# Kernel tuning notes

Hardware: AMD Instinct MI355X
Metric: run time of the kernel (lower is better)

Reference implementation:

```python
import jax, jax.numpy as jnp
import numpy as np

K = 20
EPS = 1e-6


def _vnt_linear(x, W):
    # VNT linear: rows normalized to sum to 1 (translation-equivariant channel mix)
    Wn = W / W.sum(axis=1, keepdims=True)
    return jnp.einsum('oi,bi...->bo...', Wn, x)


def _vn_lrelu(p, d):
    # Vector-neuron LeakyReLU with negative_slope=0: project p off -d half-space
    dot = jnp.sum(p * d, axis=2, keepdims=True)   # axis 2 is the 3-vector axis
    dns = jnp.sum(d * d, axis=2, keepdims=True)
    return jnp.where(dot >= 0, p, p - (dot / (dns + EPS)) * d)


def _vnt_lin_lrelu(x, W, D):
    p = _vnt_linear(x, W)
    d = jnp.einsum('oi,bi...->bo...', D, x)
    return _vn_lrelu(p, d)


def _graph_feature_cross(pts, k):
    # pts: [B, N, 3] -> edge features [B, 3(ch), 3(vec), N, k]
    B = pts.shape[0]
    xx = jnp.sum(pts * pts, axis=-1)                       # [B, N]
    inner = jnp.einsum('bnd,bmd->bnm', pts, pts)           # [B, N, N]
    pairwise = 2.0 * inner - xx[:, :, None] - xx[:, None, :]  # -||xi-xj||^2
    _, idx = jax.lax.top_k(pairwise, k)                    # [B, N, k]
    b_idx = jnp.arange(B)[:, None, None]
    nbrs = pts[b_idx, idx]                                 # [B, N, k, 3]
    ctr = jnp.broadcast_to(pts[:, :, None, :], nbrs.shape)
    cross = jnp.cross(nbrs, ctr)
    feat = jnp.stack([nbrs - ctr, ctr, cross], axis=3)     # [B, N, k, 3ch, 3vec]
    return jnp.transpose(feat, (0, 3, 4, 1, 2))            # [B, 3, 3, N, k]


def setup_inputs() -> dict:
    key = jax.random.key(0)
    ks = jax.random.split(key, 9)
    B, N, hidden = 8, 2048, 128

    def w(k_, o, i):  # positive weights -> stable row-sum normalization
        return jax.random.uniform(k_, (o, i), jnp.float32, 0.5 / i, 1.5 / i)

    def d(k_, o, i):
        return jax.random.normal(k_, (o, i), jnp.float32) / np.sqrt(i)

    return {
        'pc': jax.random.normal(ks[0], (B, N, 3), jnp.float32),
        'W_pos': w(ks[1], 64, 3), 'D_pos': d(ks[2], 64, 3),
        'W1': w(ks[3], hidden, 64), 'D1': d(ks[4], hidden, 64),
        'W2': w(ks[5], hidden, 2 * hidden), 'D2': d(ks[6], hidden, 2 * hidden),
        'W3': w(ks[7], hidden, 2 * hidden), 'D3': d(ks[8], hidden, 2 * hidden),
    }


def reference(pc, W_pos, D_pos, W1, D1, W2, D2, W3, D3):
    feat = _graph_feature_cross(pc, K)               # [B, 3, 3, N, k]
    net = _vnt_lin_lrelu(feat, W_pos, D_pos)         # [B, 64, 3, N, k]
    net = net.mean(axis=-1)                          # pool over k -> [B, 64, 3, N]
    net = _vnt_lin_lrelu(net, W1, D1)                # [B, 128, 3, N]
    pooled = jnp.broadcast_to(net.mean(axis=-1, keepdims=True), net.shape)
    net = jnp.concatenate([net, pooled], axis=1)     # [B, 256, 3, N]
    net = _vnt_lin_lrelu(net, W2, D2)                # [B, 128, 3, N]
    pooled = jnp.broadcast_to(net.mean(axis=-1, keepdims=True), net.shape)
    net = jnp.concatenate([net, pooled], axis=1)     # [B, 256, 3, N]
    net = _vnt_lin_lrelu(net, W3, D3)                # [B, 128, 3, N]
    c = net.mean(axis=-1)                            # pool over N -> [B, 128, 3]
    return c.reshape(pc.shape[0], -1)                # [B, 384]
```

## Files before the change

### kernel.cpp

```cpp
#include <hip/hip_runtime.h>
#include <hip/hip_bf16.h>
#include <math.h>

constexpr int B = 8;
constexpr int N = 2048;
constexpr int KNN = 20;
constexpr int H = 128;
constexpr int P = 3 * N;

constexpr int OSB2   = 0;
constexpr int OWT2   = 8448;
constexpr int OWT3   = 41216;
constexpr int OPS1   = 73984;
constexpr int OPS2   = 98560;
constexpr int OOUTS  = 123136;
constexpr int OBAR   = 147712;
constexpr int OSB3   = 148736;
constexpr int OWB1   = 160000;
constexpr int OWB2   = 176384;
constexpr int OWB3   = 209152;

constexpr int ZERO_BASE = OPS1;
constexpr int ZERO_CNT  = 74752;
constexpr int PREP_BLOCKS = (ZERO_CNT + 255) / 256;

constexpr int GRID_VNT  = 1024;
constexpr int BLK_PER_B = 128;

typedef __attribute__((ext_vector_type(8))) short bf16x8;
typedef __attribute__((ext_vector_type(4))) float f32x4;

__device__ __forceinline__ unsigned short f2bf(float x) {
  __hip_bfloat16 h = __float2bfloat16(x);
  return *(unsigned short*)&h;
}
__device__ __forceinline__ float bf2f(unsigned short u) {
  __hip_bfloat16 h;
  *(unsigned short*)&h = u;
  return __bfloat162float(h);
}
__device__ __forceinline__ unsigned int packhl(float x) {
  unsigned short hi = f2bf(x);
  float lo = x - bf2f(hi);
  unsigned short ls = f2bf(lo);
  return (unsigned)hi | ((unsigned)ls << 16);
}

__device__ __forceinline__ float cohload(const float* p) {
  return __hip_atomic_load(p, __ATOMIC_RELAXED, __HIP_MEMORY_SCOPE_AGENT);
}
__device__ __forceinline__ void cohstore(float* p, float v) {
  __hip_atomic_store(p, v, __ATOMIC_RELAXED, __HIP_MEMORY_SCOPE_AGENT);
}

__device__ __forceinline__ void wave_sort_key(unsigned long long& k, int lane) {
#pragma unroll
  for (int kk = 2; kk <= 64; kk <<= 1) {
#pragma unroll
    for (int j = kk >> 1; j > 0; j >>= 1) {
      unsigned long long pk =
          (unsigned long long)__shfl_xor((long long)k, j);
      bool iam_lower   = (lane & j) == 0;
      bool dir_desc    = (lane & kk) == 0;
      bool p_better    = pk > k;
      bool want_better = (dir_desc == iam_lower);
      k = (p_better == want_better) ? pk : k;
    }
  }
}

__global__ __launch_bounds__(256) void prep_kernel(
    const float* __restrict__ W1, const float* __restrict__ D1,
    const float* __restrict__ W2, const float* __restrict__ D2,
    const float* __restrict__ W3, const float* __restrict__ D3,
    float* __restrict__ ws) {
  int tid = threadIdx.x;
  int bid = blockIdx.x;
  {
    int zi = bid * 256 + tid;
    if (zi < ZERO_CNT) ws[ZERO_BASE + zi] = 0.f;
  }
  if (bid < 96) {
    int wv = tid >> 6, lane = tid & 63;
#pragma unroll
    for (int r = 0; r < 2; ++r) {
      int rr = bid * 8 + wv * 2 + r;
      const float* src;
      float* tdst = nullptr;
      unsigned int* pdst;
      int C, Cpack;
      bool norm;
      if (rr < 128)      { src = W1 + rr * 64;            C = 64;  Cpack = 64;  norm = true;
                           pdst = (unsigned int*)(ws + OWB1) + rr * 16; }
      else if (rr < 256) { int m = rr - 128; src = D1 + m * 64;  C = 64;  Cpack = 64;  norm = false;
                           pdst = (unsigned int*)(ws + OWB1) + (m + 128) * 16; }
      else if (rr < 384) { int m = rr - 256; src = W2 + m * 256; C = 256; Cpack = 128; norm = true;
                           pdst = (unsigned int*)(ws + OWB2) + m * 16; tdst = ws + OWT2 + m; }
      else if (rr < 512) { int m = rr - 384; src = D2 + m * 256; C = 256; Cpack = 128; norm = false;
                           pdst = (unsigned int*)(ws + OWB2) + (m + 128) * 16; tdst = ws + OWT2 + 128 + m; }
      else if (rr < 640) { int m = rr - 512; src = W3 + m * 256; C = 256; Cpack = 128; norm = true;
                           pdst = (unsigned int*)(ws + OWB3) + m * 16; tdst = ws + OWT3 + m; }
      else               { int m = rr - 640; src = D3 + m * 256; C = 256; Cpack = 128; norm = false;
                           pdst = (unsigned int*)(ws + OWB3) + (m + 128) * 16; tdst = ws + OWT3 + 128 + m; }
      float s = 1.f;
      if (norm) {
        float a = 0.f;
        for (int i = lane; i < C; i += 64) a += src[i];
#pragma unroll
        for (int off = 32; off > 0; off >>= 1) a += __shfl_xor(a, off);
        s = a;
      }
      for (int i = lane; i < C; i += 64) {
        float val = src[i] / s;
        if (i < Cpack) pdst[(i >> 4) * 4096 + (i & 15)] = packhl(val);
        if (tdst && i >= 128) tdst[(i - 128) * 256] = val;
      }
    }
  }
}

template <int K2, bool HASPOOL, bool LAST>
__device__ __forceinline__ void vnt_layer_body(
    unsigned short* xt, float* sb, float* spool,
    const unsigned short* __restrict__ Wb,
    const float* __restrict__ ps, const float* __restrict__ Wt,
    float* __restrict__ sbg, unsigned int* sbflag,
    float* __restrict__ pool, float* __restrict__ outs,
    unsigned int* wait_cnt, unsigned int* arrive_cnt,
    int b, int nt, int p0, int tid) {
  constexpr int KS = K2 / 32;
  constexpr int LDR = K2 + 8;
  constexpr int LDO = 132;
  float* ot = (float*)xt;
  int w = tid >> 6, lane = tid & 63;
  int q = lane >> 4, cl = lane & 15;

  bf16x8 acur[2][2], anxt[2][2];
#pragma unroll
  for (int t = 0; t < 2; ++t)
#pragma unroll
    for (int pd = 0; pd < 2; ++pd)
      acur[t][pd] = *(const bf16x8*)(Wb +
          (size_t)(32 * w + 16 * t + 128 * pd + cl) * 32 + q * 8);

  if constexpr (HASPOOL) {
    if (nt == 0) {
      if (tid == 0) {
        while (__hip_atomic_load(wait_cnt, __ATOMIC_RELAXED,
                                 __HIP_MEMORY_SCOPE_AGENT) < (unsigned)BLK_PER_B) {
          __builtin_amdgcn_s_sleep(2);
        }
      }
      __syncthreads();
      for (int i = tid; i < 384; i += 256) {
        float x = 0.f;
#pragma unroll
        for (int k = 0; k < 8; ++k)
          x += cohload(&ps[k * 3072 + b * 384 + i]);
        spool[i] = x * (1.f / 2048.f);
      }
      __syncthreads();
      float s0 = 0.f, s1 = 0.f, s2 = 0.f;
#pragma unroll 16
      for (int c = 0; c < 128; ++c) {
        float x = Wt[c * 256 + tid];
        s0 = fmaf(x, spool[c * 3 + 0], s0);
        s1 = fmaf(x, spool[c * 3 + 1], s1);
        s2 = fmaf(x, spool[c * 3 + 2], s2);
      }
      sb[tid * 3 + 0] = s0;
      sb[tid * 3 + 1] = s1;
      sb[tid * 3 + 2] = s2;
      cohstore(&sbg[tid * 3 + 0], s0);
      cohstore(&sbg[tid * 3 + 1], s1);
      cohstore(&sbg[tid * 3 + 2], s2);
      __syncthreads();
      if (tid == 0)
        __hip_atomic_fetch_add(sbflag, 1u, __ATOMIC_RELAXED,
                               __HIP_MEMORY_SCOPE_AGENT);
    } else {
      if (tid == 0) {
        while (__hip_atomic_load(sbflag, __ATOMIC_RELAXED,
                                 __HIP_MEMORY_SCOPE_AGENT) < 1u) {
          __builtin_amdgcn_s_sleep(2);
        }
      }
      __syncthreads();
      for (int i = tid; i < 768; i += 256) sb[i] = cohload(&sbg[i]);
      __syncthreads();
    }
  } else {
    __syncthreads();
  }

  f32x4 acc[2][2][3] = {};

#pragma unroll
  for (int ks = 0; ks < KS; ++ks) {
    if (ks + 1 < KS) {
#pragma unroll
      for (int t = 0; t < 2; ++t)
#pragma unroll
        for (int pd = 0; pd < 2; ++pd)
          anxt[t][pd] = *(const bf16x8*)(Wb +
              (size_t)(32 * w + 16 * t + 128 * pd + cl) * 32 + q * 8 +
              (ks + 1) * 8192);
    }
    bf16x8 bb[3];
#pragma unroll
    for (int v = 0; v < 3; ++v)
      bb[v] = *(const bf16x8*)(xt + (v * 16 + cl) * LDR + ks * 32 + q * 8);
#pragma unroll
    for (int t = 0; t < 2; ++t)
#pragma unroll
      for (int pd = 0; pd < 2; ++pd)
#pragma unroll
        for (int v = 0; v < 3; ++v)
          acc[t][pd][v] = __builtin_amdgcn_mfma_f32_16x16x32_bf16(
              acur[t][pd], bb[v], acc[t][pd][v], 0, 0, 0);
#pragma unroll
    for (int t = 0; t < 2; ++t)
#pragma unroll
      for (int pd = 0; pd < 2; ++pd)
        acur[t][pd] = anxt[t][pd];
  }
  __syncthreads();

#pragma unroll
  for (int t = 0; t < 2; ++t) {
    float res[3][4];
#pragma unroll
    for (int r = 0; r < 4; ++r) {
      int o = 32 * w + 16 * t + 4 * q + r;
      float pv[3], dvv[3];
#pragma unroll
      for (int v = 0; v < 3; ++v) {
        pv[v] = acc[t][0][v][r] + (HASPOOL ? sb[o * 3 + v] : 0.f);
        dvv[v] = acc[t][1][v][r] + (HASPOOL ? sb[(128 + o) * 3 + v] : 0.f);
      }
      float dot = fmaf(pv[0], dvv[0], fmaf(pv[1], dvv[1], pv[2] * dvv[2]));
      float dns = fmaf(dvv[0], dvv[0], fmaf(dvv[1], dvv[1], dvv[2] * dvv[2]));
      float f = (dot < 0.f) ? dot / (dns + 1e-6f) : 0.f;
#pragma unroll
      for (int v = 0; v < 3; ++v) res[v][r] = pv[v] - f * dvv[v];
    }
    int o0 = 32 * w + 16 * t + 4 * q;
#pragma unroll
    for (int v = 0; v < 3; ++v) {
      f32x4 rv = {res[v][0], res[v][1], res[v][2], res[v][3]};
      *(f32x4*)(ot + (v * 16 + cl) * LDO + o0) = rv;
    }
  }
  __syncthreads();

  int shadow = (nt & 7) * 3072;
  for (int s = tid; s < 384; s += 256) {
    int o = s / 3, v = s % 3;
    float a2 = 0.f;
#pragma unroll
    for (int c = 0; c < 16; ++c) a2 += ot[(v * 16 + c) * LDO + o];
    if (LAST) atomicAdd(outs + shadow + b * 384 + s, a2);
    else      atomicAdd(pool + shadow + b * 384 + s, a2);
  }

  __syncthreads();
  if (arrive_cnt != nullptr && tid == 0) {
    __hip_atomic_fetch_add(arrive_cnt, 1u, __ATOMIC_RELAXED,
                           __HIP_MEMORY_SCOPE_AGENT);
  }

  if constexpr (!LAST) {
    for (int s = tid; s < 1536; s += 256) {
      int pix = s >> 5, c4 = s & 31;
      float4 sv = *(float4*)(ot + pix * LDO + c4 * 4);
      uint4 vv;
      vv.x = packhl(sv.x);
      vv.y = packhl(sv.y);
      vv.z = packhl(sv.z);
      vv.w = packhl(sv.w);
      *(uint4*)(xt + pix * 264 + c4 * 8) = vv;
    }
  }
}

__global__ __launch_bounds__(256, 4) void fused_kernel(
    const float* __restrict__ pc, const float* __restrict__ Wpos,
    const float* __restrict__ Dp, float* __restrict__ ws,
    float* __restrict__ out) {
  __shared__ __align__(16) char U[35328];
  __shared__ unsigned int last_flag;
  int tid = threadIdx.x, wv = tid >> 6, lane = tid & 63;
  int bid = blockIdx.x;
  int b = bid >> 7;
  int nt = bid & 127;
  int p0 = nt * 48;

  float4* spt = (float4*)U;
  unsigned char* sph = (unsigned char*)(U + 32768) + wv * 640;
  unsigned short* sbufw = (unsigned short*)sph;
  float4* erw = (float4*)sph;
  unsigned short* xt = (unsigned short*)U;
  float* sb = (float*)(U + 25344);
  float* spool = (float*)(U + 28416);

  unsigned int* bar = (unsigned int*)(ws + OBAR);
  unsigned int* cnt1 = bar + b * 32;
  unsigned int* cnt2 = bar + 256 + b * 32;
  unsigned int* cntm = bar + 512;
  unsigned int* sbf2 = bar + 576 + b * 16;
  unsigned int* sbf3 = bar + 704 + b * 16;

  int o = lane;
  float w0 = Wpos[o * 3 + 0], w1 = Wpos[o * 3 + 1], w2 = Wpos[o * 3 + 2];
  float e0 = Dp[o * 3 + 0], e1 = Dp[o * 3 + 1], e2 = Dp[o * 3 + 2];

  const float* pcb = pc + (size_t)b * N * 3;
  for (int i = tid; i < N; i += 256) {
    float x = pcb[i * 3 + 0], y = pcb[i * 3 + 1], z = pcb[i * 3 + 2];
    float xx = __fadd_rn(__fadd_rn(__fmul_rn(x, x), __fmul_rn(y, y)), __fmul_rn(z, z));
    spt[i] = make_float4(2.f * x, 2.f * y, 2.f * z, xx);
  }
  __syncthreads();

  {
    float s = (w0 + w2) + w1;
    w0 = w0 / s; w1 = w1 / s; w2 = w2 / s;
  }

  unsigned rx0[4], rx1[4], rx2[4];

#pragma unroll
  for (int j = 0; j < 4; ++j) {
    int q = nt * 16 + wv * 4 + j;
    float4 qp = spt[q];
    float qx = 0.5f * qp.x, qy = 0.5f * qp.y, qz = 0.5f * qp.z, qxx = qp.w;

    float dv[32];
    float lmax = -INFINITY;
#pragma unroll
    for (int i = 0; i < 32; ++i) {
      float4 m = spt[i * 64 + lane];
      float A = __fadd_rn(__fadd_rn(__fmul_rn(m.x, qx), __fmul_rn(m.y, qy)),
                          __fmul_rn(m.z, qz));
      float d = __fsub_rn(__fsub_rn(A, qxx), m.w);
      dv[i] = d;
      lmax = fmaxf(lmax, d);
    }

    float sv = lmax;
#pragma unroll
    for (int k = 2; k <= 64; k <<= 1) {
#pragma unroll
      for (int jj = k >> 1; jj > 0; jj >>= 1) {
        float pv = __shfl_xor(sv, jj);
        bool keep_max = ((lane & k) == 0) == ((lane & jj) == 0);
        sv = keep_max ? fmaxf(sv, pv) : fminf(sv, pv);
      }
    }
    float tval = __shfl(sv, 19);

    unsigned msk = 0u;
#pragma unroll
    for (int i = 0; i < 32; ++i) msk |= (dv[i] >= tval) ? (1u << i) : 0u;
    int cnt = __popc(msk);
    int scan = cnt;
#pragma unroll
    for (int off = 1; off < 64; off <<= 1) {
      int t = __shfl_up(scan, off);
      scan += (lane >= off) ? t : 0;
    }
    int S = __shfl(scan, 63);
    int pos = scan - cnt;
    unsigned mm = msk;
    while (mm) {
      int i = __ffs(mm) - 1;
      mm &= mm - 1;
      if (pos < 192) sbufw[pos] = (unsigned short)(i * 64 + lane);
      ++pos;
    }

    auto distOf = [&](int m) -> float {
      float4 mp = spt[m];
      float A = __fadd_rn(__fadd_rn(__fmul_rn(mp.x, qx), __fmul_rn(mp.y, qy)),
                          __fmul_rn(mp.z, qz));
      return __fsub_rn(__fsub_rn(A, qxx), mp.w);
    };
    auto mkkey = [&](int m) -> unsigned long long {
      float d = distOf(m);
      unsigned u = __float_as_uint(d);
      u ^= (u >> 31) ? 0xFFFFFFFFu : 0x80000000u;
      return ((unsigned long long)u << 32) | (unsigned)(~m);
    };

    unsigned long long key = 0ULL;
    if (S <= 64) {
      if (lane < S) key = mkkey(sbufw[lane]);
      wave_sort_key(key, lane);
    } else if (S <= 192) {
      int p2 = 0;
      while (p2 < S) {
        if (lane >= KNN) {
          int t = p2 + lane - KNN;
          key = (t < S) ? mkkey(sbufw[t]) : 0ULL;
        }
        wave_sort_key(key, lane);
        p2 += 64 - KNN;
      }
    } else {
      int p2 = 0;
      while (p2 < N) {
        if (lane >= KNN) {
          int t = p2 + lane - KNN;
          key = (t < N) ? mkkey(t) : 0ULL;
        }
        wave_sort_key(key, lane);
        p2 += 64 - KNN;
      }
    }
    int cm = ~((unsigned)key);

    if (lane < KNN) {
      float4 t = spt[cm];
      float nx = 0.5f * t.x, ny = 0.5f * t.y, nz = 0.5f * t.z;
      float ex = nx - qx, ey = ny - qy, ez = nz - qz;
      float rrx = ny * qz - nz * qy;
      float rry = nz * qx - nx * qz;
      float rrz = nx * qy - ny * qx;
      erw[2 * lane + 0] = make_float4(ex, ey, ez, 0.f);
      erw[2 * lane + 1] = make_float4(rrx, rry, rrz, 0.f);
    }

    float cx = qx, cy = qy, cz = qz;
    float pcx = w1 * cx, pcy = w1 * cy, pcz = w1 * cz;
    float dcx = e1 * cx, dcy = e1 * cy, dcz = e1 * cz;
    float ax = 0.f, ay = 0.f, az = 0.f;
#pragma unroll 4
    for (int k = 0; k < KNN; ++k) {
      float4 e4 = erw[2 * k + 0];
      float4 r4 = erw[2 * k + 1];
      float ex = e4.x, ey = e4.y, ez = e4.z;
      float rrx = r4.x, rry = r4.y, rrz = r4.z;
      float px = fmaf(w0, ex, fmaf(w2, rrx, pcx));
      float py = fmaf(w0, ey, fmaf(w2, rry, pcy));
      float pz = fmaf(w0, ez, fmaf(w2, rrz, pcz));
      float dx = fmaf(e0, ex, fmaf(e2, rrx, dcx));
      float dy = fmaf(e0, ey, fmaf(e2, rry, dcy));
      float dz = fmaf(e0, ez, fmaf(e2, rrz, dcz));
      float dot = fmaf(px, dx, fmaf(py, dy, pz * dz));
      float dns = fmaf(dx, dx, fmaf(dy, dy, dz * dz)) + 1e-6f;
      float r0 = __builtin_amdgcn_rcpf(dns);
      r0 = r0 * fmaf(-dns, r0, 2.0f);
      float f = (dot < 0.f) ? dot * r0 : 0.f;
      ax = fmaf(-f, dx, px) + ax;
      ay = fmaf(-f, dy, py) + ay;
      az = fmaf(-f, dz, pz) + az;
    }
    rx0[j] = packhl(ax * (1.f / 20.f));
    rx1[j] = packhl(ay * (1.f / 20.f));
    rx2[j] = packhl(az * (1.f / 20.f));
  }

  __syncthreads();

#pragma unroll
  for (int j = 0; j < 4; ++j) {
    int row = wv * 4 + j;
    *(unsigned int*)(xt + (row + 0)  * 136 + 2 * o) = rx0[j];
    *(unsigned int*)(xt + (row + 16) * 136 + 2 * o) = rx1[j];
    *(unsigned int*)(xt + (row + 32) * 136 + 2 * o) = rx2[j];
  }

  vnt_layer_body<128, false, false>(
      xt, sb, spool, (const unsigned short*)(ws + OWB1),
      nullptr, nullptr, nullptr, nullptr, ws + OPS1, nullptr,
      nullptr, cnt1, b, nt, p0, tid);

  vnt_layer_body<256, true, false>(
      xt, sb, spool, (const unsigned short*)(ws + OWB2),
      ws + OPS1, ws + OWT2, ws + OSB2 + b * 768, sbf2, ws + OPS2, nullptr,
      cnt1, cnt2, b, nt, p0, tid);

  vnt_layer_body<256, true, true>(
      xt, sb, spool, (const unsigned short*)(ws + OWB3),
      ws + OPS2, ws + OWT3, ws + OSB3 + b * 768, sbf3, nullptr, ws + OOUTS,
      cnt2, nullptr, b, nt, p0, tid);

  if (tid == 0) {
    unsigned old = __hip_atomic_fetch_add(cntm, 1u, __ATOMIC_RELAXED,
                                          __HIP_MEMORY_SCOPE_AGENT);
    last_flag = (old == (unsigned)GRID_VNT - 1) ? 1u : 0u;
  }
  __syncthreads();
  if (last_flag) {
    const float* outs = ws + OOUTS;
    for (int idx = tid; idx < B * 384; idx += 256) {
      float s = 0.f;
#pragma unroll
      for (int k = 0; k < 8; ++k) s += cohload(&outs[k * 3072 + idx]);
      out[idx] = s * (1.f / 2048.f);
    }
  }
}

extern "C" void kernel_launch(void* const* d_in, const int* in_sizes, int n_in,
                              void* d_out, int out_size, void* d_ws, size_t ws_size,
                              hipStream_t stream) {
  (void)in_sizes; (void)n_in; (void)out_size; (void)ws_size;
  const float* pc   = (const float*)d_in[0];
  const float* Wpos = (const float*)d_in[1];
  const float* Dpos = (const float*)d_in[2];
  const float* W1   = (const float*)d_in[3];
  const float* D1   = (const float*)d_in[4];
  const float* W2   = (const float*)d_in[5];
  const float* D2   = (const float*)d_in[6];
  const float* W3   = (const float*)d_in[7];
  const float* D3   = (const float*)d_in[8];
  float* out = (float*)d_out;
  float* ws  = (float*)d_ws;

  prep_kernel<<<PREP_BLOCKS, 256, 0, stream>>>(W1, D1, W2, D2, W3, D3, ws);

  fused_kernel<<<GRID_VNT, 256, 0, stream>>>(pc, Wpos, Dpos, ws, out);
}
```

Before: 157.3 us.

## Double block size to 512 threads, halving per-wave work in kNN and MFMA layers

```diff
diff --git a/kernel.cpp b/kernel.cpp
--- a/kernel.cpp
+++ b/kernel.cpp
@@ -135,13 +135,11 @@
   int w = tid >> 6, lane = tid & 63;
   int q = lane >> 4, cl = lane & 15;
 
-  bf16x8 acur[2][2], anxt[2][2];
-#pragma unroll
-  for (int t = 0; t < 2; ++t)
-#pragma unroll
-    for (int pd = 0; pd < 2; ++pd)
-      acur[t][pd] = *(const bf16x8*)(Wb +
-          (size_t)(32 * w + 16 * t + 128 * pd + cl) * 32 + q * 8);
+  bf16x8 acur[2], anxt[2];
+#pragma unroll
+  for (int pd = 0; pd < 2; ++pd)
+    acur[pd] = *(const bf16x8*)(Wb +
+        (size_t)(16 * w + 128 * pd + cl) * 32 + q * 8);
 
   if constexpr (HASPOOL) {
     if (nt == 0) {
@@ -152,7 +150,7 @@
         }
       }
       __syncthreads();
-      for (int i = tid; i < 384; i += 256) {
+      for (int i = tid; i < 384; i += 512) {
         float x = 0.f;
 #pragma unroll
         for (int k = 0; k < 8; ++k)
@@ -160,20 +158,22 @@
         spool[i] = x * (1.f / 2048.f);
       }
       __syncthreads();
-      float s0 = 0.f, s1 = 0.f, s2 = 0.f;
+      if (tid < 256) {
+        float s0 = 0.f, s1 = 0.f, s2 = 0.f;
 #pragma unroll 16
-      for (int c = 0; c < 128; ++c) {
-        float x = Wt[c * 256 + tid];
-        s0 = fmaf(x, spool[c * 3 + 0], s0);
-        s1 = fmaf(x, spool[c * 3 + 1], s1);
-        s2 = fmaf(x, spool[c * 3 + 2], s2);
-      }
-      sb[tid * 3 + 0] = s0;
-      sb[tid * 3 + 1] = s1;
-      sb[tid * 3 + 2] = s2;
-      cohstore(&sbg[tid * 3 + 0], s0);
-      cohstore(&sbg[tid * 3 + 1], s1);
-      cohstore(&sbg[tid * 3 + 2], s2);
+        for (int c = 0; c < 128; ++c) {
+          float x = Wt[c * 256 + tid];
+          s0 = fmaf(x, spool[c * 3 + 0], s0);
+          s1 = fmaf(x, spool[c * 3 + 1], s1);
+          s2 = fmaf(x, spool[c * 3 + 2], s2);
+        }
+        sb[tid * 3 + 0] = s0;
+        sb[tid * 3 + 1] = s1;
+        sb[tid * 3 + 2] = s2;
+        cohstore(&sbg[tid * 3 + 0], s0);
+        cohstore(&sbg[tid * 3 + 1], s1);
+        cohstore(&sbg[tid * 3 + 2], s2);
+      }
       __syncthreads();
       if (tid == 0)
         __hip_atomic_fetch_add(sbflag, 1u, __ATOMIC_RELAXED,
@@ -186,57 +186,50 @@
         }
       }
       __syncthreads();
-      for (int i = tid; i < 768; i += 256) sb[i] = cohload(&sbg[i]);
+      for (int i = tid; i < 768; i += 512) sb[i] = cohload(&sbg[i]);
       __syncthreads();
     }
   } else {
     __syncthreads();
   }
 
-  f32x4 acc[2][2][3] = {};
+  f32x4 acc[2][3] = {};
 
 #pragma unroll
   for (int ks = 0; ks < KS; ++ks) {
     if (ks + 1 < KS) {
 #pragma unroll
-      for (int t = 0; t < 2; ++t)
-#pragma unroll
-        for (int pd = 0; pd < 2; ++pd)
-          anxt[t][pd] = *(const bf16x8*)(Wb +
-              (size_t)(32 * w + 16 * t + 128 * pd + cl) * 32 + q * 8 +
-              (ks + 1) * 8192);
+      for (int pd = 0; pd < 2; ++pd)
+        anxt[pd] = *(const bf16x8*)(Wb +
+            (size_t)(16 * w + 128 * pd + cl) * 32 + q * 8 +
+            (ks + 1) * 8192);
     }
     bf16x8 bb[3];
 #pragma unroll
     for (int v = 0; v < 3; ++v)
       bb[v] = *(const bf16x8*)(xt + (v * 16 + cl) * LDR + ks * 32 + q * 8);
 #pragma unroll
-    for (int t = 0; t < 2; ++t)
-#pragma unroll
-      for (int pd = 0; pd < 2; ++pd)
-#pragma unroll
-        for (int v = 0; v < 3; ++v)
-          acc[t][pd][v] = __builtin_amdgcn_mfma_f32_16x16x32_bf16(
-              acur[t][pd], bb[v], acc[t][pd][v], 0, 0, 0);
-#pragma unroll
-    for (int t = 0; t < 2; ++t)
-#pragma unroll
-      for (int pd = 0; pd < 2; ++pd)
-        acur[t][pd] = anxt[t][pd];
+    for (int pd = 0; pd < 2; ++pd)
+#pragma unroll
+      for (int v = 0; v < 3; ++v)
+        acc[pd][v] = __builtin_amdgcn_mfma_f32_16x16x32_bf16(
+            acur[pd], bb[v], acc[pd][v], 0, 0, 0);
+#pragma unroll
+    for (int pd = 0; pd < 2; ++pd)
+      acur[pd] = anxt[pd];
   }
   __syncthreads();
 
-#pragma unroll
-  for (int t = 0; t < 2; ++t) {
+  {
     float res[3][4];
 #pragma unroll
     for (int r = 0; r < 4; ++r) {
-      int o = 32 * w + 16 * t + 4 * q + r;
+      int o = 16 * w + 4 * q + r;
       float pv[3], dvv[3];
 #pragma unroll
       for (int v = 0; v < 3; ++v) {
-        pv[v] = acc[t][0][v][r] + (HASPOOL ? sb[o * 3 + v] : 0.f);
-        dvv[v] = acc[t][1][v][r] + (HASPOOL ? sb[(128 + o) * 3 + v] : 0.f);
+        pv[v] = acc[0][v][r] + (HASPOOL ? sb[o * 3 + v] : 0.f);
+        dvv[v] = acc[1][v][r] + (HASPOOL ? sb[(128 + o) * 3 + v] : 0.f);
       }
       float dot = fmaf(pv[0], dvv[0], fmaf(pv[1], dvv[1], pv[2] * dvv[2]));
       float dns = fmaf(dvv[0], dvv[0], fmaf(dvv[1], dvv[1], dvv[2] * dvv[2]));
@@ -244,7 +237,7 @@
 #pragma unroll
       for (int v = 0; v < 3; ++v) res[v][r] = pv[v] - f * dvv[v];
     }
-    int o0 = 32 * w + 16 * t + 4 * q;
+    int o0 = 16 * w + 4 * q;
 #pragma unroll
     for (int v = 0; v < 3; ++v) {
       f32x4 rv = {res[v][0], res[v][1], res[v][2], res[v][3]};
@@ -254,7 +247,7 @@
   __syncthreads();
 
   int shadow = (nt & 7) * 3072;
-  for (int s = tid; s < 384; s += 256) {
+  for (int s = tid; s < 384; s += 512) {
     int o = s / 3, v = s % 3;
     float a2 = 0.f;
 #pragma unroll
@@ -270,7 +263,7 @@
   }
 
   if constexpr (!LAST) {
-    for (int s = tid; s < 1536; s += 256) {
+    for (int s = tid; s < 1536; s += 512) {
       int pix = s >> 5, c4 = s & 31;
       float4 sv = *(float4*)(ot + pix * LDO + c4 * 4);
       uint4 vv;
@@ -283,11 +276,11 @@
   }
 }
 
-__global__ __launch_bounds__(256, 4) void fused_kernel(
+__global__ __launch_bounds__(512, 8) void fused_kernel(
     const float* __restrict__ pc, const float* __restrict__ Wpos,
     const float* __restrict__ Dp, float* __restrict__ ws,
     float* __restrict__ out) {
-  __shared__ __align__(16) char U[35328];
+  __shared__ __align__(16) char U[37888];
   __shared__ unsigned int last_flag;
   int tid = threadIdx.x, wv = tid >> 6, lane = tid & 63;
   int bid = blockIdx.x;
@@ -315,7 +308,7 @@
   float e0 = Dp[o * 3 + 0], e1 = Dp[o * 3 + 1], e2 = Dp[o * 3 + 2];
 
   const float* pcb = pc + (size_t)b * N * 3;
-  for (int i = tid; i < N; i += 256) {
+  for (int i = tid; i < N; i += 512) {
     float x = pcb[i * 3 + 0], y = pcb[i * 3 + 1], z = pcb[i * 3 + 2];
     float xx = __fadd_rn(__fadd_rn(__fmul_rn(x, x), __fmul_rn(y, y)), __fmul_rn(z, z));
     spt[i] = make_float4(2.f * x, 2.f * y, 2.f * z, xx);
@@ -327,11 +320,11 @@
     w0 = w0 / s; w1 = w1 / s; w2 = w2 / s;
   }
 
-  unsigned rx0[4], rx1[4], rx2[4];
-
-#pragma unroll
-  for (int j = 0; j < 4; ++j) {
-    int q = nt * 16 + wv * 4 + j;
+  unsigned rx0[2], rx1[2], rx2[2];
+
+#pragma unroll
+  for (int j = 0; j < 2; ++j) {
+    int q = nt * 16 + wv * 2 + j;
     float4 qp = spt[q];
     float qx = 0.5f * qp.x, qy = 0.5f * qp.y, qz = 0.5f * qp.z, qxx = qp.w;
 
@@ -463,8 +456,8 @@
   __syncthreads();
 
 #pragma unroll
-  for (int j = 0; j < 4; ++j) {
-    int row = wv * 4 + j;
+  for (int j = 0; j < 2; ++j) {
+    int row = wv * 2 + j;
     *(unsigned int*)(xt + (row + 0)  * 136 + 2 * o) = rx0[j];
     *(unsigned int*)(xt + (row + 16) * 136 + 2 * o) = rx1[j];
     *(unsigned int*)(xt + (row + 32) * 136 + 2 * o) = rx2[j];
@@ -493,7 +486,7 @@
   __syncthreads();
   if (last_flag) {
     const float* outs = ws + OOUTS;
-    for (int idx = tid; idx < B * 384; idx += 256) {
+    for (int idx = tid; idx < B * 384; idx += 512) {
       float s = 0.f;
 #pragma unroll
       for (int k = 0; k < 8; ++k) s += cohload(&outs[k * 3072 + idx]);
@@ -520,5 +513,5 @@
 
   prep_kernel<<<PREP_BLOCKS, 256, 0, stream>>>(W1, D1, W2, D2, W3, D3, ws);
 
-  fused_kernel<<<GRID_VNT, 256, 0, stream>>>(pc, Wpos, Dpos, ws, out);
-}
+  fused_kernel<<<GRID_VNT, 512, 0, stream>>>(pc, Wpos, Dpos, ws, out);
+}
```

Result: slower. 192.9 us (+22.6%).

## Replace atomic pooled reductions with per-block slots and per-batch finalization

Applied to the files above, without the earlier changes.

```diff
diff --git a/kernel.cpp b/kernel.cpp
--- a/kernel.cpp
+++ b/kernel.cpp
@@ -11,18 +11,17 @@
 constexpr int OSB2   = 0;
 constexpr int OWT2   = 8448;
 constexpr int OWT3   = 41216;
-constexpr int OPS1   = 73984;
-constexpr int OPS2   = 98560;
-constexpr int OOUTS  = 123136;
 constexpr int OBAR   = 147712;
 constexpr int OSB3   = 148736;
 constexpr int OWB1   = 160000;
 constexpr int OWB2   = 176384;
 constexpr int OWB3   = 209152;
-
-constexpr int ZERO_BASE = OPS1;
-constexpr int ZERO_CNT  = 74752;
-constexpr int PREP_BLOCKS = (ZERO_CNT + 255) / 256;
+constexpr int OPS1   = 250000;
+constexpr int OPS2   = 650000;
+constexpr int OOUTS  = 1050000;
+
+constexpr int ZERO_BASE = OBAR;
+constexpr int ZERO_CNT  = 1024;
 
 constexpr int GRID_VNT  = 1024;
 constexpr int BLK_PER_B = 128;
@@ -125,7 +124,7 @@
     const unsigned short* __restrict__ Wb,
     const float* __restrict__ ps, const float* __restrict__ Wt,
     float* __restrict__ sbg, unsigned int* sbflag,
-    float* __restrict__ pool, float* __restrict__ outs,
+    float* __restrict__ dstslots,
     unsigned int* wait_cnt, unsigned int* arrive_cnt,
     int b, int nt, int p0, int tid) {
   constexpr int KS = K2 / 32;
@@ -154,9 +153,8 @@
       __syncthreads();
       for (int i = tid; i < 384; i += 256) {
         float x = 0.f;
-#pragma unroll
-        for (int k = 0; k < 8; ++k)
-          x += cohload(&ps[k * 3072 + b * 384 + i]);
+        for (int k = 0; k < BLK_PER_B; ++k)
+          x += cohload(&ps[(size_t)(b * BLK_PER_B + k) * 384 + i]);
         spool[i] = x * (1.f / 2048.f);
       }
       __syncthreads();
@@ -253,14 +251,15 @@
   }
   __syncthreads();
 
-  int shadow = (nt & 7) * 3072;
-  for (int s = tid; s < 384; s += 256) {
-    int o = s / 3, v = s % 3;
-    float a2 = 0.f;
-#pragma unroll
-    for (int c = 0; c < 16; ++c) a2 += ot[(v * 16 + c) * LDO + o];
-    if (LAST) atomicAdd(outs + shadow + b * 384 + s, a2);
-    else      atomicAdd(pool + shadow + b * 384 + s, a2);
+  {
+    float* myslot = dstslots + (size_t)(b * BLK_PER_B + nt) * 384;
+    for (int s = tid; s < 384; s += 256) {
+      int o = s / 3, v = s % 3;
+      float a2 = 0.f;
+#pragma unroll
+      for (int c = 0; c < 16; ++c) a2 += ot[(v * 16 + c) * LDO + o];
+      cohstore(&myslot[s], a2);
+    }
   }
 
   __syncthreads();
@@ -306,9 +305,9 @@
   unsigned int* bar = (unsigned int*)(ws + OBAR);
   unsigned int* cnt1 = bar + b * 32;
   unsigned int* cnt2 = bar + 256 + b * 32;
-  unsigned int* cntm = bar + 512;
-  unsigned int* sbf2 = bar + 576 + b * 16;
-  unsigned int* sbf3 = bar + 704 + b * 16;
+  unsigned int* cnt3 = bar + 512 + b * 32;
+  unsigned int* sbf2 = bar + 768 + b * 16;
+  unsigned int* sbf3 = bar + 896 + b * 16;
 
   int o = lane;
   float w0 = Wpos[o * 3 + 0], w1 = Wpos[o * 3 + 1], w2 = Wpos[o * 3 + 2];
@@ -472,32 +471,31 @@
 
   vnt_layer_body<128, false, false>(
       xt, sb, spool, (const unsigned short*)(ws + OWB1),
-      nullptr, nullptr, nullptr, nullptr, ws + OPS1, nullptr,
+      nullptr, nullptr, nullptr, nullptr, ws + OPS1,
       nullptr, cnt1, b, nt, p0, tid);
 
   vnt_layer_body<256, true, false>(
       xt, sb, spool, (const unsigned short*)(ws + OWB2),
-      ws + OPS1, ws + OWT2, ws + OSB2 + b * 768, sbf2, ws + OPS2, nullptr,
+      ws + OPS1, ws + OWT2, ws + OSB2 + b * 768, sbf2, ws + OPS2,
       cnt1, cnt2, b, nt, p0, tid);
 
   vnt_layer_body<256, true, true>(
       xt, sb, spool, (const unsigned short*)(ws + OWB3),
-      ws + OPS2, ws + OWT3, ws + OSB3 + b * 768, sbf3, nullptr, ws + OOUTS,
+      ws + OPS2, ws + OWT3, ws + OSB3 + b * 768, sbf3, ws + OOUTS,
       cnt2, nullptr, b, nt, p0, tid);
 
   if (tid == 0) {
-    unsigned old = __hip_atomic_fetch_add(cntm, 1u, __ATOMIC_RELAXED,
+    unsigned old = __hip_atomic_fetch_add(cnt3, 1u, __ATOMIC_RELAXED,
                                           __HIP_MEMORY_SCOPE_AGENT);
-    last_flag = (old == (unsigned)GRID_VNT - 1) ? 1u : 0u;
+    last_flag = (old == (unsigned)BLK_PER_B - 1) ? 1u : 0u;
   }
   __syncthreads();
   if (last_flag) {
-    const float* outs = ws + OOUTS;
-    for (int idx = tid; idx < B * 384; idx += 256) {
+    const float* ob = ws + OOUTS + (size_t)b * BLK_PER_B * 384;
+    for (int idx = tid; idx < 384; idx += 256) {
       float s = 0.f;
-#pragma unroll
-      for (int k = 0; k < 8; ++k) s += cohload(&outs[k * 3072 + idx]);
-      out[idx] = s * (1.f / 2048.f);
+      for (int k = 0; k < BLK_PER_B; ++k) s += cohload(&ob[k * 384 + idx]);
+      out[b * 384 + idx] = s * (1.f / 2048.f);
     }
   }
 }
@@ -518,7 +516,7 @@
   float* out = (float*)d_out;
   float* ws  = (float*)d_ws;
 
-  prep_kernel<<<PREP_BLOCKS, 256, 0, stream>>>(W1, D1, W2, D2, W3, D3, ws);
+  prep_kernel<<<96, 256, 0, stream>>>(W1, D1, W2, D2, W3, D3, ws);
 
   fused_kernel<<<GRID_VNT, 256, 0, stream>>>(pc, Wpos, Dpos, ws, out);
 }
```

New measurement: 198.8 us. +26.4%, slower.
